# Performance work log

Measured on AMD Instinct MI355X. Metric: run time of the kernel, lower is better.

Reference implementation:

```python
import math
import jax, jax.numpy as jnp
import numpy as np

EPS = 1e-8
N_ITER = 5


def _partial_ot(C, reg):
    # C: (M, N) cost matrix. Faithful to partial_optimal_transport with
    # diag-matmuls replaced by equivalent broadcast row/col scaling.
    M, N = C.shape
    a = jnp.full((M,), 1.0 / M, dtype=C.dtype)
    b = jnp.full((N,), 1.0 / N, dtype=C.dtype)
    m = jnp.minimum(a.sum(), b.sum())  # = 1.0 here
    K = jnp.exp(-C / jnp.clip(reg, EPS))
    K = K * (m / jnp.clip(K.sum(), EPS))

    def body(K, _):
        r = jnp.minimum(a / jnp.clip(K.sum(axis=1), EPS), 1.0)   # min(a/rowsum, dx)
        K1 = r[:, None] * K
        c = jnp.minimum(b / jnp.clip(K1.sum(axis=0), EPS), 1.0)  # min(b/colsum, dy)
        K2 = K1 * c[None, :]
        K = K2 * (m / jnp.clip(K2.sum(), EPS))
        return K, None

    K, _ = jax.lax.scan(body, K, None, length=N_ITER)
    return K


def _rigid_transform(a, b, w):
    # a: (M,3) source points, b: (M,3) weighted targets, w: (M,) weights
    wn = w[:, None] / (w.sum() + 1e-6)            # normalized weights (M,1)
    centroid_a = (a * wn).sum(axis=0)             # (3,)
    centroid_b = (b * wn).sum(axis=0)
    ac = a - centroid_a
    bc = b - centroid_b
    cov = ac.T @ (bc * wn)                        # (3,3)
    u, s, vh = jnp.linalg.svd(cov, full_matrices=False)
    v = vh.T                                      # torch.svd's V
    rot_pos = v @ u.T
    v_neg = v.at[:, 2].multiply(-1.0)
    rot_neg = v_neg @ u.T
    det = jnp.linalg.det(rot_pos)
    rot = jnp.where(det > 0, rot_pos, rot_neg)
    trans = -rot @ centroid_a + centroid_b        # (3,)
    return jnp.concatenate([rot, trans[:, None]], axis=1)  # (3,4)


def _one_sample(se, te, s, t, rho):
    # se: (D,M) src feats, te: (D,N) tgt feats, s: (3,M), t: (3,N)
    D = se.shape[0]
    scores = (se.T @ te) / math.sqrt(D)           # (M,N)
    C = -jax.nn.log_softmax(scores, axis=1)
    matches = _partial_ot(C, rho)                 # (M,N)
    rowsum = matches.sum(axis=1, keepdims=True)   # (M,1)
    weighted_ref = (matches @ t.T) / (rowsum + 1e-6)  # (M,3)
    T = _rigid_transform(s.T, weighted_ref, rowsum[:, 0])
    return T, matches


def _forward(src_embedding, tgt_embedding, src, tgt, rho):
    Ts, match_mats = jax.vmap(_one_sample, in_axes=(0, 0, 0, 0, None))(
        src_embedding, tgt_embedding, src, tgt, rho)
    return Ts[:, :3, :3], Ts[:, :3, 3], match_mats


def setup_inputs() -> dict:
    key = jax.random.key(0)
    k1, k2, k3, k4 = jax.random.split(key, 4)
    B, D, M, N = 16, 256, 2048, 2048
    return {
        "src_embedding": jax.random.normal(k1, (B, D, M), dtype=jnp.float32),
        "tgt_embedding": jax.random.normal(k2, (B, D, N), dtype=jnp.float32),
        "src": jax.random.normal(k3, (B, 3, M), dtype=jnp.float32),
        "tgt": jax.random.normal(k4, (B, 3, N), dtype=jnp.float32),
        "rho": jnp.asarray(1.0, dtype=jnp.float32),
    }


def reference(src_embedding, tgt_embedding, src, tgt, rho):
    return _forward(src_embedding, tgt_embedding, src, tgt, rho)
```

## Files before the change

kernel.cpp:

```cpp
#include <hip/hip_runtime.h>
#include <math.h>

#define B_ 16
#define D_ 256
#define M_ 2048
#define N_ 2048
#define EPSF 1e-8f
#define AVAL (1.0f/2048.0f)

typedef __bf16  bf16x8 __attribute__((ext_vector_type(8)));
typedef float   f32x4  __attribute__((ext_vector_type(4)));

__device__ __forceinline__ float wredsum(float x){
  #pragma unroll
  for (int off=32; off; off>>=1) x += __shfl_xor(x, off);
  return x;
}
__device__ __forceinline__ float wredmax(float x){
  #pragma unroll
  for (int off=32; off; off>>=1) x = fmaxf(x, __shfl_xor(x, off));
  return x;
}
__device__ __forceinline__ unsigned short f2bf(float x){
  unsigned int v = __float_as_uint(x);
  unsigned int r = (v + 0x7fffu + ((v>>16)&1u)) >> 16;
  return (unsigned short)r;
}
__device__ __forceinline__ float bf2f(unsigned short u){ return __uint_as_float(((unsigned int)u)<<16); }
__device__ __forceinline__ float h2f(unsigned short h){
  _Float16 x; __builtin_memcpy(&x,&h,2); return (float)x;
}
__device__ __forceinline__ unsigned short f2h(float x){
  _Float16 h = (_Float16)x; unsigned short u; __builtin_memcpy(&u,&h,2); return u;
}

__device__ __forceinline__ void gll16(const void* gsrc, void* ldst){
  __builtin_amdgcn_global_load_lds(
      (const __attribute__((address_space(1))) unsigned int*)gsrc,
      (__attribute__((address_space(3))) unsigned int*)(unsigned int)(unsigned long long)ldst,
      16, 0, 0);
}

__global__ __launch_bounds__(256) void convert_kernel(const float* __restrict__ se,
                                                      const float* __restrict__ te,
                                                      uint4* __restrict__ Ah, uint4* __restrict__ Al,
                                                      uint4* __restrict__ Bh, uint4* __restrict__ Bl)
{
  const int t  = threadIdx.x;
  const int mb = blockIdx.x;
  const int g  = blockIdx.y;
  const int z  = blockIdx.z;
  const int b  = z & 15, op = z >> 4;
  const int m  = mb*256 + t;
  const float* src = (op ? te : se) + (size_t)b*D_*M_ + (size_t)g*8*M_ + m;
  float x[8];
  #pragma unroll
  for (int j=0;j<8;j++) x[j] = src[(size_t)j*M_];
  unsigned int hw[4], lw[4];
  #pragma unroll
  for (int p=0;p<4;p++){
    float a0 = x[2*p], a1 = x[2*p+1];
    unsigned short h0 = f2bf(a0), h1 = f2bf(a1);
    unsigned short q0 = f2bf(a0 - bf2f(h0)), q1 = f2bf(a1 - bf2f(h1));
    hw[p] = (unsigned)h0 | ((unsigned)h1<<16);
    lw[p] = (unsigned)q0 | ((unsigned)q1<<16);
  }
  const size_t gi = (size_t)(b*32 + g)*2048 + m;
  uint4* Ph = op ? Bh : Ah;
  uint4* Pl = op ? Bl : Al;
  Ph[gi] = *(const uint4*)hw;
  Pl[gi] = *(const uint4*)lw;
}

__global__ __launch_bounds__(256) void gemm_fast(const uint4* __restrict__ Ah,
                                                 const uint4* __restrict__ Al,
                                                 const uint4* __restrict__ Bh,
                                                 const uint4* __restrict__ Bl,
                                                 float* __restrict__ S)
{
  __shared__ unsigned int sAh[2048], sAl[2048], sBh[2048], sBl[2048];
  const int b  = blockIdx.z;
  const int mb = blockIdx.y;
  const int nb = blockIdx.x;
  const int t    = threadIdx.x;
  const int wave = t >> 6, lane = t & 63;
  const int wy = wave >> 1, wx = wave & 1;
  const int quad = lane >> 4, l15 = lane & 15;

  f32x4 acc[4][4] = {};

  for (int kc=0; kc<8; kc++){
    __syncthreads();
    #pragma unroll
    for (int r=0;r<2;r++){
      const int i  = r*256 + t;
      const int gq = i >> 7, m = i & 127;
      const size_t rowg = (size_t)(b*32 + kc*4 + gq)*2048;
      gll16(Ah + rowg + mb*128 + m, (char*)sAh + (size_t)i*16);
      gll16(Al + rowg + mb*128 + m, (char*)sAl + (size_t)i*16);
      gll16(Bh + rowg + nb*128 + m, (char*)sBh + (size_t)i*16);
      gll16(Bl + rowg + nb*128 + m, (char*)sBl + (size_t)i*16);
    }
    __syncthreads();
    bf16x8 ah[4], al[4], bh[4], bl[4];
    #pragma unroll
    for (int rt=0;rt<4;rt++){
      int ra = (quad*128 + wy*64 + rt*16 + l15)*4;
      int rb = (quad*128 + wx*64 + rt*16 + l15)*4;
      ah[rt] = *(const bf16x8*)&sAh[ra];
      al[rt] = *(const bf16x8*)&sAl[ra];
      bh[rt] = *(const bf16x8*)&sBh[rb];
      bl[rt] = *(const bf16x8*)&sBl[rb];
    }
    #pragma unroll
    for (int rt=0;rt<4;rt++)
      #pragma unroll
      for (int ct=0;ct<4;ct++){
        acc[rt][ct] = __builtin_amdgcn_mfma_f32_16x16x32_bf16(ah[rt], bh[ct], acc[rt][ct], 0,0,0);
        acc[rt][ct] = __builtin_amdgcn_mfma_f32_16x16x32_bf16(ah[rt], bl[ct], acc[rt][ct], 0,0,0);
        acc[rt][ct] = __builtin_amdgcn_mfma_f32_16x16x32_bf16(al[rt], bh[ct], acc[rt][ct], 0,0,0);
      }
  }
  const float sc = 0.0625f;
  #pragma unroll
  for (int rt=0;rt<4;rt++){
    #pragma unroll
    for (int r=0;r<4;r++){
      int m = mb*128 + wy*64 + rt*16 + quad*4 + r;
      float* rowp = S + (size_t)(b*M_ + m)*N_;
      #pragma unroll
      for (int ct=0;ct<4;ct++){
        int n = nb*128 + wx*64 + ct*16 + l15;
        rowp[n] = acc[rt][ct][r] * sc;
      }
    }
  }
}

__global__ __launch_bounds__(256) void gemm_kernel(const float* __restrict__ se,
                                                   const float* __restrict__ te,
                                                   float* __restrict__ S)
{
  __shared__ unsigned int Ah[2048], Al[2048], Bh[2048], Bl[2048];
  const int b  = blockIdx.z;
  const int mb = blockIdx.y;
  const int nb = blockIdx.x;
  const int t    = threadIdx.x;
  const int wave = t >> 6, lane = t & 63;
  const int wy = wave >> 1, wx = wave & 1;
  const int quad = lane >> 4, l15 = lane & 15;
  const int ml  = t & 127;
  const int dh  = t >> 7;

  f32x4 acc[4][4] = {};

  const float* Abase = se + (size_t)b*D_*M_ + mb*128 + ml;
  const float* Bbase = te + (size_t)b*D_*M_ + nb*128 + ml;

  for (int kc=0; kc<8; kc++){
    __syncthreads();
    {
      float x[16];
      #pragma unroll
      for (int j=0;j<16;j++) x[j] = Abase[(size_t)(kc*32 + dh*16 + j)*M_];
      #pragma unroll
      for (int gi=0; gi<2; gi++){
        unsigned int hw[4], lw[4];
        #pragma unroll
        for (int p=0;p<4;p++){
          float a0 = x[gi*8+2*p], a1 = x[gi*8+2*p+1];
          unsigned short h0 = f2bf(a0), h1 = f2bf(a1);
          unsigned short q0 = f2bf(a0 - bf2f(h0)), q1 = f2bf(a1 - bf2f(h1));
          hw[p] = (unsigned)h0 | ((unsigned)h1<<16);
          lw[p] = (unsigned)q0 | ((unsigned)q1<<16);
        }
        int idx = ((dh*2+gi)*128 + ml)*4;
        *(uint4*)&Ah[idx] = *(uint4*)hw;
        *(uint4*)&Al[idx] = *(uint4*)lw;
      }
    }
    {
      float x[16];
      #pragma unroll
      for (int j=0;j<16;j++) x[j] = Bbase[(size_t)(kc*32 + dh*16 + j)*M_];
      #pragma unroll
      for (int gi=0; gi<2; gi++){
        unsigned int hw[4], lw[4];
        #pragma unroll
        for (int p=0;p<4;p++){
          float a0 = x[gi*8+2*p], a1 = x[gi*8+2*p+1];
          unsigned short h0 = f2bf(a0), h1 = f2bf(a1);
          unsigned short q0 = f2bf(a0 - bf2f(h0)), q1 = f2bf(a1 - bf2f(h1));
          hw[p] = (unsigned)h0 | ((unsigned)h1<<16);
          lw[p] = (unsigned)q0 | ((unsigned)q1<<16);
        }
        int idx = ((dh*2+gi)*128 + ml)*4;
        *(uint4*)&Bh[idx] = *(uint4*)hw;
        *(uint4*)&Bl[idx] = *(uint4*)lw;
      }
    }
    __syncthreads();
    bf16x8 ah[4], al[4], bh[4], bl[4];
    #pragma unroll
    for (int rt=0;rt<4;rt++){
      int ra = (quad*128 + wy*64 + rt*16 + l15)*4;
      int rb = (quad*128 + wx*64 + rt*16 + l15)*4;
      ah[rt] = *(const bf16x8*)&Ah[ra];
      al[rt] = *(const bf16x8*)&Al[ra];
      bh[rt] = *(const bf16x8*)&Bh[rb];
      bl[rt] = *(const bf16x8*)&Bl[rb];
    }
    #pragma unroll
    for (int rt=0;rt<4;rt++)
      #pragma unroll
      for (int ct=0;ct<4;ct++){
        acc[rt][ct] = __builtin_amdgcn_mfma_f32_16x16x32_bf16(ah[rt], bh[ct], acc[rt][ct], 0,0,0);
        acc[rt][ct] = __builtin_amdgcn_mfma_f32_16x16x32_bf16(ah[rt], bl[ct], acc[rt][ct], 0,0,0);
        acc[rt][ct] = __builtin_amdgcn_mfma_f32_16x16x32_bf16(al[rt], bh[ct], acc[rt][ct], 0,0,0);
      }
  }
  const float sc = 0.0625f;
  #pragma unroll
  for (int rt=0;rt<4;rt++){
    #pragma unroll
    for (int r=0;r<4;r++){
      int m = mb*128 + wy*64 + rt*16 + quad*4 + r;
      float* rowp = S + (size_t)(b*M_ + m)*N_;
      #pragma unroll
      for (int ct=0;ct<4;ct++){
        int n = nb*128 + wx*64 + ct*16 + l15;
        rowp[n] = acc[rt][ct][r] * sc;
      }
    }
  }
}

__global__ __launch_bounds__(256) void stats_kernel(float* __restrict__ S,
                                                    const float* __restrict__ rho,
                                                    float* __restrict__ lse,
                                                    float* __restrict__ y0)
{
  const int b = blockIdx.y;
  const int m = blockIdx.x*4 + (threadIdx.x>>6);
  const int lane = threadIdx.x & 63;
  const float invrho = 1.0f / fmaxf(rho[0], EPSF);
  float* row = S + (size_t)(b*M_ + m)*N_;
  const float4* row4 = (const float4*)row;
  float4 vals[8];
  float mx = -3.4e38f;
  #pragma unroll
  for (int k=0;k<8;k++){
    float4 v = row4[lane + 64*k];
    vals[k] = v;
    mx = fmaxf(mx, fmaxf(fmaxf(v.x,v.y), fmaxf(v.z,v.w)));
  }
  mx = wredmax(mx);
  float e1=0.0f;
  #pragma unroll
  for (int k=0;k<8;k++){
    float4 v = vals[k];
    e1 += __expf(v.x-mx)+__expf(v.y-mx)+__expf(v.z-mx)+__expf(v.w-mx);
  }
  e1 = wredsum(e1);
  const float l = mx + __logf(e1);
  uint2* rowh2 = (uint2*)row;
  float y2 = 0.0f;
  #pragma unroll
  for (int k=0;k<8;k++){
    float4 v = vals[k];
    unsigned short h0 = f2h(__expf((v.x-l)*invrho));
    unsigned short h1 = f2h(__expf((v.y-l)*invrho));
    unsigned short h2 = f2h(__expf((v.z-l)*invrho));
    unsigned short h3 = f2h(__expf((v.w-l)*invrho));
    y2 += h2f(h0)+h2f(h1)+h2f(h2)+h2f(h3);
    uint2 pk;
    pk.x = (unsigned)h0 | ((unsigned)h1<<16);
    pk.y = (unsigned)h2 | ((unsigned)h3<<16);
    rowh2[lane + 64*k] = pk;
  }
  y2 = wredsum(y2);
  if (lane==0){
    lse[b*M_+m] = l;
    y0 [b*M_+m] = y2;
  }
}

__global__ __launch_bounds__(256) void init_kernel(const float* __restrict__ y0,
                                                   float* __restrict__ u, float* __restrict__ v,
                                                   float* __restrict__ w, float* __restrict__ g)
{
  const int b = blockIdx.x; const int t = threadIdx.x;
  float s = 0.0f;
  for (int i=t;i<M_;i+=256) s += y0[b*M_+i];
  s = wredsum(s);
  __shared__ float red[4];
  __shared__ float gsh;
  if ((t&63)==0) red[t>>6]=s;
  __syncthreads();
  if (t==0){
    float tot = red[0]+red[1]+red[2]+red[3];
    float gg = 1.0f / fmaxf(tot, EPSF);
    g[b]=gg; gsh=gg;
  }
  __syncthreads();
  float gg = gsh;
  for (int i=t;i<M_;i+=256){
    float rs = gg * y0[b*M_+i];
    u[b*M_+i] = fminf(AVAL / fmaxf(rs, EPSF), 1.0f);
    v[b*M_+i] = 1.0f;
    w[b*M_+i] = 0.0f;
  }
}

__global__ __launch_bounds__(256) void row_kernel(const float* __restrict__ S,
                                                  const float* __restrict__ vv,
                                                  float* __restrict__ u,
                                                  const float* __restrict__ g)
{
  const int b = blockIdx.y;
  const int m = blockIdx.x*4 + (threadIdx.x>>6);
  const int lane = threadIdx.x & 63;
  const uint4*  rowh = (const uint4*)(S + (size_t)(b*M_ + m)*N_);
  const float4* vp   = (const float4*)(vv + (size_t)b*N_);
  float acc=0.0f;
  #pragma unroll
  for (int k=0;k<4;k++){
    uint4 su = rowh[lane + 64*k];
    float4 v0 = vp[(lane+64*k)*2];
    float4 v1 = vp[(lane+64*k)*2+1];
    acc += h2f((unsigned short)(su.x&0xffff))*v0.x + h2f((unsigned short)(su.x>>16))*v0.y
         + h2f((unsigned short)(su.y&0xffff))*v0.z + h2f((unsigned short)(su.y>>16))*v0.w
         + h2f((unsigned short)(su.z&0xffff))*v1.x + h2f((unsigned short)(su.z>>16))*v1.y
         + h2f((unsigned short)(su.w&0xffff))*v1.z + h2f((unsigned short)(su.w>>16))*v1.w;
  }
  acc = wredsum(acc);
  if (lane==0){
    float ui = u[b*M_+m];
    float rs = g[b]*ui*acc;
    u[b*M_+m] = ui * fminf(AVAL / fmaxf(rs, EPSF), 1.0f);
  }
}

__global__ __launch_bounds__(256) void col_kernel(const float* __restrict__ S,
                                                  const float* __restrict__ u,
                                                  float* __restrict__ w)
{
  const int b  = blockIdx.y;
  const int i0 = blockIdx.x*64;
  const int t  = threadIdx.x;
  float acc[8];
  #pragma unroll
  for (int k=0;k<8;k++) acc[k]=0.0f;
  for (int i=0;i<64;i++){
    int r = i0+i;
    float ui = u[b*M_+r];
    uint4 su = ((const uint4*)(S + (size_t)(b*M_ + r)*N_))[t];
    acc[0] += ui*h2f((unsigned short)(su.x&0xffff));
    acc[1] += ui*h2f((unsigned short)(su.x>>16));
    acc[2] += ui*h2f((unsigned short)(su.y&0xffff));
    acc[3] += ui*h2f((unsigned short)(su.y>>16));
    acc[4] += ui*h2f((unsigned short)(su.z&0xffff));
    acc[5] += ui*h2f((unsigned short)(su.z>>16));
    acc[6] += ui*h2f((unsigned short)(su.w&0xffff));
    acc[7] += ui*h2f((unsigned short)(su.w>>16));
  }
  #pragma unroll
  for (int k=0;k<8;k++) atomicAdd(&w[b*N_+t*8+k], acc[k]);
}

__global__ __launch_bounds__(256) void vupd_kernel(float* __restrict__ w,
                                                   float* __restrict__ v,
                                                   float* __restrict__ g)
{
  const int b = blockIdx.x; const int t = threadIdx.x;
  const float gg = g[b];
  float part = 0.0f;
  for (int i=t;i<N_;i+=256){
    float wj = w[b*N_+i];
    float vj = v[b*N_+i];
    float c  = fminf(AVAL/fmaxf(gg*vj*wj,EPSF), 1.0f);
    vj *= c;
    v[b*N_+i]=vj;
    part += wj*vj;
    w[b*N_+i]=0.0f;
  }
  part = wredsum(part);
  __shared__ float red[4];
  if ((t&63)==0) red[t>>6]=part;
  __syncthreads();
  if (t==0){
    float tot = gg*(red[0]+red[1]+red[2]+red[3]);
    g[b] = gg / fmaxf(tot, EPSF);
  }
}

__global__ __launch_bounds__(256) void final_kernel(float* __restrict__ S,
                                                    const float* __restrict__ u,
                                                    const float* __restrict__ v,
                                                    const float* __restrict__ g,
                                                    const float* __restrict__ tgt,
                                                    float* __restrict__ rowsum,
                                                    float* __restrict__ wref)
{
  const int b = blockIdx.y;
  const int m = blockIdx.x*4 + (threadIdx.x>>6);
  const int lane = threadIdx.x & 63;
  const float gu = g[b]*u[b*M_+m];
  float* row = S + (size_t)(b*M_ + m)*N_;
  const uint4* rowh = (const uint4*)row;
  uint4 su[4];
  #pragma unroll
  for (int k=0;k<4;k++) su[k] = rowh[lane + 64*k];
  __builtin_amdgcn_s_waitcnt(0);
  float4* rowf = (float4*)row;
  const float4* vp = (const float4*)(v + (size_t)b*N_);
  const float4* t0 = (const float4*)(tgt + ((size_t)b*3+0)*N_);
  const float4* t1 = (const float4*)(tgt + ((size_t)b*3+1)*N_);
  const float4* t2 = (const float4*)(tgt + ((size_t)b*3+2)*N_);
  float rs=0.0f, a0=0.0f, a1=0.0f, a2=0.0f;
  #pragma unroll
  for (int k=0;k<4;k++){
    float s[8] = {h2f((unsigned short)(su[k].x&0xffff)), h2f((unsigned short)(su[k].x>>16)),
                  h2f((unsigned short)(su[k].y&0xffff)), h2f((unsigned short)(su[k].y>>16)),
                  h2f((unsigned short)(su[k].z&0xffff)), h2f((unsigned short)(su[k].z>>16)),
                  h2f((unsigned short)(su[k].w&0xffff)), h2f((unsigned short)(su[k].w>>16))};
    int i2 = (lane+64*k)*2;
    #pragma unroll
    for (int h=0;h<2;h++){
      float4 v4 = vp[i2+h];
      float4 q0 = t0[i2+h], q1 = t1[i2+h], q2 = t2[i2+h];
      float m0 = gu*s[h*4+0]*v4.x;
      float m1 = gu*s[h*4+1]*v4.y;
      float m2 = gu*s[h*4+2]*v4.z;
      float m3 = gu*s[h*4+3]*v4.w;
      rs += m0+m1+m2+m3;
      a0 += m0*q0.x + m1*q0.y + m2*q0.z + m3*q0.w;
      a1 += m0*q1.x + m1*q1.y + m2*q1.z + m3*q1.w;
      a2 += m0*q2.x + m1*q2.y + m2*q2.z + m3*q2.w;
      rowf[i2+h] = make_float4(m0,m1,m2,m3);
    }
  }
  rs = wredsum(rs); a0=wredsum(a0); a1=wredsum(a1); a2=wredsum(a2);
  if (lane==0){
    rowsum[b*M_+m] = rs;
    float inv = 1.0f/(rs+1e-6f);
    size_t o = ((size_t)b*M_+m)*3;
    wref[o]=a0*inv; wref[o+1]=a1*inv; wref[o+2]=a2*inv;
  }
}

__device__ __forceinline__ void mat3_svd_rot(const float cov[3][3], float R[3][3])
{
  float mx = 1e-30f;
  for (int p=0;p<3;p++) for (int q=0;q<3;q++) mx = fmaxf(mx, fabsf(cov[p][q]));
  const float inv = 1.0f/mx;
  float Cm[3][3];
  for (int p=0;p<3;p++) for (int q=0;q<3;q++) Cm[p][q]=cov[p][q]*inv;
  float G[3][3];
  for (int p=0;p<3;p++)
    for (int q=0;q<3;q++)
      G[p][q] = Cm[0][p]*Cm[0][q] + Cm[1][p]*Cm[1][q] + Cm[2][p]*Cm[2][q];
  float V[3][3] = {{1,0,0},{0,1,0},{0,0,1}};
  const int PP[3]={0,0,1}, QQ[3]={1,2,2};
  for (int sweep=0;sweep<12;sweep++){
    for (int r=0;r<3;r++){
      int p=PP[r], q=QQ[r];
      float apq = G[p][q];
      if (fabsf(apq) < 1e-20f) continue;
      float tau = (G[q][q]-G[p][p])/(2.0f*apq);
      float tt  = (tau>=0.0f?1.0f:-1.0f)/(fabsf(tau)+sqrtf(1.0f+tau*tau));
      float cc  = 1.0f/sqrtf(1.0f+tt*tt);
      float ss  = tt*cc;
      for (int k=0;k<3;k++){ float gkp=G[k][p], gkq=G[k][q]; G[k][p]=cc*gkp-ss*gkq; G[k][q]=ss*gkp+cc*gkq; }
      for (int k=0;k<3;k++){ float gpk=G[p][k], gqk=G[q][k]; G[p][k]=cc*gpk-ss*gqk; G[q][k]=ss*gpk+cc*gqk; }
      for (int k=0;k<3;k++){ float vkp=V[k][p], vkq=V[k][q]; V[k][p]=cc*vkp-ss*vkq; V[k][q]=ss*vkp+cc*vkq; }
    }
  }
  float ev[3]={G[0][0],G[1][1],G[2][2]};
  int i0=0,i1=1,i2=2,tmp;
  if (ev[i0]<ev[i1]){tmp=i0;i0=i1;i1=tmp;}
  if (ev[i0]<ev[i2]){tmp=i0;i0=i2;i2=tmp;}
  if (ev[i1]<ev[i2]){tmp=i1;i1=i2;i2=tmp;}
  const int idx[3]={i0,i1,i2};
  float Vs[3][3];
  for (int k=0;k<3;k++) for (int i=0;i<3;i++) Vs[i][k]=V[i][idx[k]];
  float U[3][3]; float nrm[3];
  for (int k=0;k<3;k++){
    float ux = Cm[0][0]*Vs[0][k]+Cm[0][1]*Vs[1][k]+Cm[0][2]*Vs[2][k];
    float uy = Cm[1][0]*Vs[0][k]+Cm[1][1]*Vs[1][k]+Cm[1][2]*Vs[2][k];
    float uz = Cm[2][0]*Vs[0][k]+Cm[2][1]*Vs[1][k]+Cm[2][2]*Vs[2][k];
    float n = sqrtf(ux*ux+uy*uy+uz*uz);
    nrm[k]=n;
    float in = (n>1e-20f)?1.0f/n:0.0f;
    U[0][k]=ux*in; U[1][k]=uy*in; U[2][k]=uz*in;
  }
  if (nrm[2] < 1e-6f*fmaxf(nrm[0],1e-20f)){
    U[0][2]=U[1][0]*U[2][1]-U[2][0]*U[1][1];
    U[1][2]=U[2][0]*U[0][1]-U[0][0]*U[2][1];
    U[2][2]=U[0][0]*U[1][1]-U[1][0]*U[0][1];
  }
  float detC = Cm[0][0]*(Cm[1][1]*Cm[2][2]-Cm[1][2]*Cm[2][1])
             - Cm[0][1]*(Cm[1][0]*Cm[2][2]-Cm[1][2]*Cm[2][0])
             + Cm[0][2]*(Cm[1][0]*Cm[2][1]-Cm[1][1]*Cm[2][0]);
  float d2 = (detC>0.0f)?1.0f:-1.0f;
  for (int p=0;p<3;p++)
    for (int q=0;q<3;q++)
      R[p][q] = Vs[p][0]*U[q][0] + Vs[p][1]*U[q][1] + d2*Vs[p][2]*U[q][2];
}

__global__ __launch_bounds__(256) void rigid_kernel(const float* __restrict__ src,
                                                    const float* __restrict__ wref,
                                                    const float* __restrict__ rowsum,
                                                    float* __restrict__ out)
{
  const int b = blockIdx.x; const int t = threadIdx.x;
  float acc[16];
  #pragma unroll
  for (int k=0;k<16;k++) acc[k]=0.0f;
  for (int i=t;i<M_;i+=256){
    float wgt = rowsum[b*M_+i];
    float ax = src[((size_t)b*3+0)*M_+i];
    float ay = src[((size_t)b*3+1)*M_+i];
    float az = src[((size_t)b*3+2)*M_+i];
    const float* wr = wref + ((size_t)b*M_+i)*3;
    float bx=wr[0], by=wr[1], bz=wr[2];
    acc[0]+=wgt;
    acc[1]+=wgt*ax; acc[2]+=wgt*ay; acc[3]+=wgt*az;
    acc[4]+=wgt*bx; acc[5]+=wgt*by; acc[6]+=wgt*bz;
    acc[7] +=wgt*ax*bx; acc[8] +=wgt*ax*by; acc[9] +=wgt*ax*bz;
    acc[10]+=wgt*ay*bx; acc[11]+=wgt*ay*by; acc[12]+=wgt*ay*bz;
    acc[13]+=wgt*az*bx; acc[14]+=wgt*az*by; acc[15]+=wgt*az*bz;
  }
  __shared__ float red[4][16];
  const int wid = t>>6, lane = t&63;
  #pragma unroll
  for (int k=0;k<16;k++){
    float v = acc[k];
    #pragma unroll
    for (int off=32; off; off>>=1) v += __shfl_xor(v, off);
    if (lane==0) red[wid][k]=v;
  }
  __syncthreads();
  if (t==0){
    float s[16];
    #pragma unroll
    for (int k=0;k<16;k++) s[k]=red[0][k]+red[1][k]+red[2][k]+red[3][k];
    float wsum = s[0];
    float denom = wsum + 1e-6f;
    float ca[3]={s[1]/denom, s[2]/denom, s[3]/denom};
    float cb[3]={s[4]/denom, s[5]/denom, s[6]/denom};
    float sw = wsum/denom;
    float cov[3][3];
    for (int p=0;p<3;p++)
      for (int q=0;q<3;q++)
        cov[p][q] = s[7+p*3+q]/denom + (sw-2.0f)*ca[p]*cb[q];
    float R[3][3];
    mat3_svd_rot(cov, R);
    float tr[3];
    for (int p=0;p<3;p++)
      tr[p] = -(R[p][0]*ca[0]+R[p][1]*ca[1]+R[p][2]*ca[2]) + cb[p];
    for (int p=0;p<3;p++)
      for (int q=0;q<3;q++)
        out[b*9 + p*3 + q] = R[p][q];
    for (int p=0;p<3;p++)
      out[144 + b*3 + p] = tr[p];
  }
}

extern "C" void kernel_launch(void* const* d_in, const int* in_sizes, int n_in,
                              void* d_out, int out_size, void* d_ws, size_t ws_size,
                              hipStream_t stream)
{
  const float* se  = (const float*)d_in[0];
  const float* te  = (const float*)d_in[1];
  const float* src = (const float*)d_in[2];
  const float* tgt = (const float*)d_in[3];
  const float* rho = (const float*)d_in[4];
  float* out = (float*)d_out;
  float* S   = out + 192;
  float* ws  = (float*)d_ws;
  float* lse = ws;
  float* y0  = ws + 32768;
  float* u   = ws + 65536;
  float* v   = ws + 98304;
  float* w   = ws + 131072;
  float* g   = ws + 163840;
  float* wref= ws + 163904;

  const size_t PLANE_G     = (size_t)16*32*2048;
  const size_t PLANE_BYTES = PLANE_G*16;
  const size_t PLANE_OFF   = 1048832;
  const size_t need        = PLANE_OFF + 4*PLANE_BYTES;

  if (ws_size >= need){
    uint4* Ah = (uint4*)((char*)d_ws + PLANE_OFF);
    uint4* Al = Ah + PLANE_G;
    uint4* Bh = Al + PLANE_G;
    uint4* Bl = Bh + PLANE_G;
    convert_kernel<<<dim3(8,32,32),256,0,stream>>>(se,te,Ah,Al,Bh,Bl);
    gemm_fast     <<<dim3(16,16,16),256,0,stream>>>(Ah,Al,Bh,Bl,S);
  } else {
    gemm_kernel   <<<dim3(16,16,16),256,0,stream>>>(se,te,S);
  }
  stats_kernel<<<dim3(512,16),  256,0,stream>>>(S,rho,lse,y0);
  init_kernel <<<dim3(16),      256,0,stream>>>(y0,u,v,w,g);
  for (int it=0; it<5; ++it){
    if (it>0) row_kernel<<<dim3(512,16),256,0,stream>>>(S,v,u,g);
    col_kernel <<<dim3(32,16),256,0,stream>>>(S,u,w);
    vupd_kernel<<<dim3(16),   256,0,stream>>>(w,v,g);
  }
  final_kernel<<<dim3(512,16),256,0,stream>>>(S,u,v,g,tgt,y0,wref);
  rigid_kernel<<<dim3(16),    256,0,stream>>>(src,wref,y0,out);
}
```

Measured before the change: 923.0 us.

## Fuse Sinkhorn row-scaling and column-sum passes into one kernel

```diff
diff --git a/kernel.cpp b/kernel.cpp
--- a/kernel.cpp
+++ b/kernel.cpp
@@ -312,35 +312,6 @@
   }
 }
 
-__global__ __launch_bounds__(256) void row_kernel(const float* __restrict__ S,
-                                                  const float* __restrict__ vv,
-                                                  float* __restrict__ u,
-                                                  const float* __restrict__ g)
-{
-  const int b = blockIdx.y;
-  const int m = blockIdx.x*4 + (threadIdx.x>>6);
-  const int lane = threadIdx.x & 63;
-  const uint4*  rowh = (const uint4*)(S + (size_t)(b*M_ + m)*N_);
-  const float4* vp   = (const float4*)(vv + (size_t)b*N_);
-  float acc=0.0f;
-  #pragma unroll
-  for (int k=0;k<4;k++){
-    uint4 su = rowh[lane + 64*k];
-    float4 v0 = vp[(lane+64*k)*2];
-    float4 v1 = vp[(lane+64*k)*2+1];
-    acc += h2f((unsigned short)(su.x&0xffff))*v0.x + h2f((unsigned short)(su.x>>16))*v0.y
-         + h2f((unsigned short)(su.y&0xffff))*v0.z + h2f((unsigned short)(su.y>>16))*v0.w
-         + h2f((unsigned short)(su.z&0xffff))*v1.x + h2f((unsigned short)(su.z>>16))*v1.y
-         + h2f((unsigned short)(su.w&0xffff))*v1.z + h2f((unsigned short)(su.w>>16))*v1.w;
-  }
-  acc = wredsum(acc);
-  if (lane==0){
-    float ui = u[b*M_+m];
-    float rs = g[b]*ui*acc;
-    u[b*M_+m] = ui * fminf(AVAL / fmaxf(rs, EPSF), 1.0f);
-  }
-}
-
 __global__ __launch_bounds__(256) void col_kernel(const float* __restrict__ S,
                                                   const float* __restrict__ u,
                                                   float* __restrict__ w)
@@ -366,6 +337,71 @@
   }
   #pragma unroll
   for (int k=0;k<8;k++) atomicAdd(&w[b*N_+t*8+k], acc[k]);
+}
+
+__global__ __launch_bounds__(256) void fused_rc_kernel(const float* __restrict__ S,
+                                                       const float* __restrict__ vv,
+                                                       float* __restrict__ u,
+                                                       float* __restrict__ w,
+                                                       const float* __restrict__ g)
+{
+  __shared__ float wsh[4][2048];
+  const int b   = blockIdx.y;
+  const int i0  = blockIdx.x*64;
+  const int t   = threadIdx.x;
+  const int wid = t>>6, lane = t&63;
+  const float gg = g[b];
+  const float4* vp = (const float4*)(vv + (size_t)b*N_);
+
+  float acc[32];
+  #pragma unroll
+  for (int k=0;k<32;k++) acc[k]=0.0f;
+
+  for (int r=0;r<16;r++){
+    const int m = i0 + wid*16 + r;
+    const uint4* rowh = (const uint4*)(S + (size_t)(b*M_ + m)*N_);
+    float sv[32];
+    float dot = 0.0f;
+    #pragma unroll
+    for (int k=0;k<4;k++){
+      uint4 su  = rowh[lane + 64*k];
+      float4 v0 = vp[(lane+64*k)*2];
+      float4 v1 = vp[(lane+64*k)*2+1];
+      float s0 = h2f((unsigned short)(su.x&0xffff));
+      float s1 = h2f((unsigned short)(su.x>>16));
+      float s2 = h2f((unsigned short)(su.y&0xffff));
+      float s3 = h2f((unsigned short)(su.y>>16));
+      float s4 = h2f((unsigned short)(su.z&0xffff));
+      float s5 = h2f((unsigned short)(su.z>>16));
+      float s6 = h2f((unsigned short)(su.w&0xffff));
+      float s7 = h2f((unsigned short)(su.w>>16));
+      dot += s0*v0.x + s1*v0.y + s2*v0.z + s3*v0.w
+           + s4*v1.x + s5*v1.y + s6*v1.z + s7*v1.w;
+      sv[k*8+0]=s0; sv[k*8+1]=s1; sv[k*8+2]=s2; sv[k*8+3]=s3;
+      sv[k*8+4]=s4; sv[k*8+5]=s5; sv[k*8+6]=s6; sv[k*8+7]=s7;
+    }
+    dot = wredsum(dot);
+    float ui = u[b*M_+m];
+    float rs = gg*ui*dot;
+    float un = ui * fminf(AVAL / fmaxf(rs, EPSF), 1.0f);
+    if (lane==0) u[b*M_+m] = un;
+    #pragma unroll
+    for (int k=0;k<32;k++) acc[k] += un * sv[k];
+  }
+
+  #pragma unroll
+  for (int k=0;k<4;k++){
+    #pragma unroll
+    for (int e=0;e<8;e++)
+      wsh[wid][(lane+64*k)*8+e] = acc[k*8+e];
+  }
+  __syncthreads();
+  #pragma unroll
+  for (int e=0;e<8;e++){
+    int j = t*8+e;
+    float s = wsh[0][j]+wsh[1][j]+wsh[2][j]+wsh[3][j];
+    atomicAdd(&w[b*N_+j], s);
+  }
 }
 
 __global__ __launch_bounds__(256) void vupd_kernel(float* __restrict__ w,
@@ -604,10 +640,11 @@
   }
   stats_kernel<<<dim3(512,16),  256,0,stream>>>(S,rho,lse,y0);
   init_kernel <<<dim3(16),      256,0,stream>>>(y0,u,v,w,g);
-  for (int it=0; it<5; ++it){
-    if (it>0) row_kernel<<<dim3(512,16),256,0,stream>>>(S,v,u,g);
-    col_kernel <<<dim3(32,16),256,0,stream>>>(S,u,w);
-    vupd_kernel<<<dim3(16),   256,0,stream>>>(w,v,g);
+  col_kernel <<<dim3(32,16),256,0,stream>>>(S,u,w);
+  vupd_kernel<<<dim3(16),   256,0,stream>>>(w,v,g);
+  for (int it=1; it<5; ++it){
+    fused_rc_kernel<<<dim3(32,16),256,0,stream>>>(S,v,u,w,g);
+    vupd_kernel    <<<dim3(16),   256,0,stream>>>(w,v,g);
   }
   final_kernel<<<dim3(512,16),256,0,stream>>>(S,u,v,g,tgt,y0,wref);
   rigid_kernel<<<dim3(16),    256,0,stream>>>(src,wref,y0,out);
```

After: 835.4 us. 9.5% less time.
